# Kernel tuning notes

Hardware: AMD Instinct MI355X
Metric: run time of the kernel (lower is better)

## Reference

```python
import jax, jax.numpy as jnp
import numpy as np

EPS = 1e-12


def _sn(w, u):
    """One power-iteration step of spectral norm (eval mode: u not updated).
    w: [out, in] (1x1 conv weight viewed as matrix); u: [1, out].
    u/v are computed without gradient (torch no_grad), but sv = v W^T u^T
    carries gradient through w, matching the source.
    """
    v = u @ w  # [1, in]
    v = v / jnp.maximum(jnp.linalg.norm(v), EPS)
    v = jax.lax.stop_gradient(v)
    u2 = v @ w.T  # [1, out]
    u2 = u2 / jnp.maximum(jnp.linalg.norm(u2), EPS)
    u2 = jax.lax.stop_gradient(u2)
    sv = (v @ w.T @ u2.T)[0, 0]
    return w / sv


def _conv1x1(x, w):
    # x: [B,C,H,W], w: [O,C] -> [B,O,H,W]
    return jnp.einsum('oc,bchw->bohw', w, x)


def _maxpool2(x):
    B, C, H, W = x.shape
    return x.reshape(B, C, H // 2, 2, W // 2, 2).max(axis=(3, 5))


def setup_inputs() -> dict:
    key = jax.random.key(0)
    ks = jax.random.split(key, 10)
    B, C, H, W = 8, 512, 64, 64
    return {
        'x': jax.random.normal(ks[0], (B, C, H, W), jnp.float32),
        'w_theta': jax.random.normal(ks[1], (C // 8, C), jnp.float32) * 0.05,
        'w_phi': jax.random.normal(ks[2], (C // 8, C), jnp.float32) * 0.05,
        'w_g': jax.random.normal(ks[3], (C // 2, C), jnp.float32) * 0.05,
        'w_o': jax.random.normal(ks[4], (C, C // 2), jnp.float32) * 0.05,
        'u_theta': jax.random.normal(ks[5], (1, C // 8), jnp.float32),
        'u_phi': jax.random.normal(ks[6], (1, C // 8), jnp.float32),
        'u_g': jax.random.normal(ks[7], (1, C // 2), jnp.float32),
        'u_o': jax.random.normal(ks[8], (1, C), jnp.float32),
        'gamma': jax.random.normal(ks[9], (), jnp.float32),
    }


def reference(x, w_theta, w_phi, w_g, w_o, u_theta, u_phi, u_g, u_o, gamma):
    B, C, H, W = x.shape
    theta = _conv1x1(x, _sn(w_theta, u_theta))               # [B, C/8, H, W]
    phi = _maxpool2(_conv1x1(x, _sn(w_phi, u_phi)))          # [B, C/8, H/2, W/2]
    g = _maxpool2(_conv1x1(x, _sn(w_g, u_g)))                # [B, C/2, H/2, W/2]
    theta = theta.reshape(B, C // 8, H * W)
    phi = phi.reshape(B, C // 8, H * W // 4)
    g = g.reshape(B, C // 2, H * W // 4)
    # attention: [B, HW, HW/4]
    beta = jax.nn.softmax(jnp.einsum('bcn,bcm->bnm', theta, phi), axis=-1)
    o = jnp.einsum('bcm,bnm->bcn', g, beta).reshape(B, C // 2, H, W)
    o = _conv1x1(o, _sn(w_o, u_o))                           # [B, C, H, W]
    return gamma * o + x
```

## Files before the change

kernel.cpp:

```cpp
#include <hip/hip_runtime.h>
#include <math.h>

#define NB 8
#define NC 512
#define CK 64
#define CG 256
#define NPIX 4096
#define MPIX 1024

#define OFF_WT 0u
#define OFF_WP 32768u
#define OFF_WG 65536u
#define OFF_WO 196608u
#define OFF_TH 327680u
#define OFF_PH 2424832u
#define OFF_G  2949120u
#define OFF_OA 5046272u

__global__ __launch_bounds__(256) void sn_kernel(
    const float* __restrict__ w_theta, const float* __restrict__ w_phi,
    const float* __restrict__ w_g, const float* __restrict__ w_o,
    const float* __restrict__ u_theta, const float* __restrict__ u_phi,
    const float* __restrict__ u_g, const float* __restrict__ u_o,
    float* __restrict__ ws) {
  const int which = blockIdx.x;
  const float* w; const float* u; int outn, inn; float* dst;
  if (which == 0)      { w = w_theta; u = u_theta; outn = 64;  inn = 512; dst = ws + OFF_WT; }
  else if (which == 1) { w = w_phi;   u = u_phi;   outn = 64;  inn = 512; dst = ws + OFF_WP; }
  else if (which == 2) { w = w_g;     u = u_g;     outn = 256; inn = 512; dst = ws + OFF_WG; }
  else                 { w = w_o;     u = u_o;     outn = 512; inn = 256; dst = ws + OFF_WO; }
  __shared__ float us[512];
  __shared__ float vs[512];
  __shared__ float red[256];
  const int t = threadIdx.x;
  for (int i = t; i < outn; i += 256) us[i] = u[i];
  __syncthreads();
  float v0 = 0.f, v1 = 0.f;
  const int i0 = t, i1 = t + 256;
  for (int o = 0; o < outn; ++o) {
    const float* wr = w + (size_t)o * inn;
    const float uo = us[o];
    v0 += uo * wr[i0];
    if (i1 < inn) v1 += uo * wr[i1];
  }
  float ss = v0 * v0 + ((i1 < inn) ? v1 * v1 : 0.f);
  red[t] = ss;
  __syncthreads();
  for (int s2 = 128; s2 > 0; s2 >>= 1) { if (t < s2) red[t] += red[t + s2]; __syncthreads(); }
  const float vnorm = fmaxf(sqrtf(red[0]), 1e-12f);
  const float vinv = 1.f / vnorm;
  vs[i0] = v0 * vinv;
  if (i1 < inn) vs[i1] = v1 * vinv;
  __syncthreads();
  float ss2 = 0.f;
  for (int o = t; o < outn; o += 256) {
    const float* wr = w + (size_t)o * inn;
    float s = 0.f;
    for (int i = 0; i < inn; ++i) s += wr[i] * vs[i];
    ss2 += s * s;
  }
  red[t] = ss2;
  __syncthreads();
  for (int s2 = 128; s2 > 0; s2 >>= 1) { if (t < s2) red[t] += red[t + s2]; __syncthreads(); }
  const float sv = fmaxf(sqrtf(red[0]), 1e-12f);
  const float inv = 1.f / sv;
  const int total = outn * inn;
  for (int k = t; k < total; k += 256) dst[k] = w[k] * inv;
}

__global__ __launch_bounds__(256) void qkv_gemm(
    const float* __restrict__ x, const float* __restrict__ wcat,
    float* __restrict__ th_out, float* __restrict__ ph_out, float* __restrict__ g_out) {
  const int b = blockIdx.z;
  const int m0 = blockIdx.y * 128;
  const int n0 = blockIdx.x * 128;
  const int t = threadIdx.x;
  const int tx = t & 15, ty = t >> 4;
  __shared__ float As[16][128];
  __shared__ float Bs[16][128];
  float acc[8][8];
#pragma unroll
  for (int r = 0; r < 8; ++r)
#pragma unroll
    for (int j = 0; j < 8; ++j) acc[r][j] = 0.f;
  const float* xb = x + (size_t)b * NC * NPIX;
  const int am = t >> 1, ak = (t & 1) * 8;
  const int bk = t >> 4, bn = (t & 15) * 8;
  const float* aptr = wcat + (size_t)(m0 + am) * 512 + ak;
  const float* bptr = xb + (size_t)bk * NPIX + n0 + bn;
  float4 a0 = *(const float4*)(aptr);
  float4 a1 = *(const float4*)(aptr + 4);
  float4 b0 = *(const float4*)(bptr);
  float4 b1 = *(const float4*)(bptr + 4);
  for (int k0 = 0; k0 < 512; k0 += 16) {
    __syncthreads();
    As[ak + 0][am] = a0.x; As[ak + 1][am] = a0.y; As[ak + 2][am] = a0.z; As[ak + 3][am] = a0.w;
    As[ak + 4][am] = a1.x; As[ak + 5][am] = a1.y; As[ak + 6][am] = a1.z; As[ak + 7][am] = a1.w;
    *(float4*)&Bs[bk][bn] = b0;
    *(float4*)&Bs[bk][bn + 4] = b1;
    __syncthreads();
    if (k0 + 16 < 512) {
      a0 = *(const float4*)(aptr + k0 + 16);
      a1 = *(const float4*)(aptr + k0 + 20);
      b0 = *(const float4*)(bptr + (size_t)(k0 + 16) * NPIX);
      b1 = *(const float4*)(bptr + (size_t)(k0 + 16) * NPIX + 4);
    }
#pragma unroll
    for (int kk = 0; kk < 16; ++kk) {
      float4 av0 = *(float4*)&As[kk][ty * 4];
      float4 av1 = *(float4*)&As[kk][ty * 4 + 64];
      float4 bv0 = *(float4*)&Bs[kk][tx * 4];
      float4 bv1 = *(float4*)&Bs[kk][tx * 4 + 64];
      float a[8] = {av0.x, av0.y, av0.z, av0.w, av1.x, av1.y, av1.z, av1.w};
      float bb[8] = {bv0.x, bv0.y, bv0.z, bv0.w, bv1.x, bv1.y, bv1.z, bv1.w};
#pragma unroll
      for (int r = 0; r < 8; ++r)
#pragma unroll
        for (int j = 0; j < 8; ++j) acc[r][j] = fmaf(a[r], bb[j], acc[r][j]);
    }
  }
  const int hp = n0 >> 7;
#pragma unroll
  for (int r = 0; r < 8; ++r) {
    const int ch = m0 + ty * 4 + (r & 3) + ((r >= 4) ? 64 : 0);
    if (ch < 64) {
      float4 v0 = {acc[r][0], acc[r][1], acc[r][2], acc[r][3]};
      float4 v1 = {acc[r][4], acc[r][5], acc[r][6], acc[r][7]};
      float* dst = th_out + ((size_t)(b * CK + ch)) * NPIX + n0;
      *(float4*)(dst + tx * 4) = v0;
      *(float4*)(dst + 64 + tx * 4) = v1;
    } else {
      const float p0 = fmaxf(fmaxf(acc[r][0], acc[r][1]), fmaxf(acc[r][4], acc[r][5]));
      const float p1 = fmaxf(fmaxf(acc[r][2], acc[r][3]), fmaxf(acc[r][6], acc[r][7]));
      float* dst;
      if (ch < 128) dst = ph_out + ((size_t)(b * CK + (ch - 64))) * MPIX + hp * 32 + tx * 2;
      else          dst = g_out  + ((size_t)(b * CG + (ch - 128))) * MPIX + hp * 32 + tx * 2;
      float2 pv = {p0, p1};
      *(float2*)dst = pv;
    }
  }
}

__global__ __launch_bounds__(256) void attn_kernel(
    const float* __restrict__ th, const float* __restrict__ ph,
    const float* __restrict__ gg, float* __restrict__ oat) {
  const int b = blockIdx.x & 7;
  const int n0 = (blockIdx.x >> 3) * 64;
  const int t = threadIdx.x;
  const int tx = t & 15, tg = t >> 4;
  __shared__ float sth[64][64];
  __shared__ float buf[2][64][64];
  __shared__ float seb[64][64];
  __shared__ float sden[64];
  {
    const float* src = th + (size_t)b * CK * NPIX + n0;
    for (int idx = t; idx < 1024; idx += 256) {
      int c = idx >> 4, q = (idx & 15) << 2;
      *(float4*)&sth[c][q] = *(const float4*)(src + (size_t)c * NPIX + q);
    }
  }
  const float* phb = ph + (size_t)b * CK * MPIX;
  const float* ggb = gg + (size_t)b * CG * MPIX;
  const int c0 = t >> 4;
  const int q0 = (t & 15) << 2;
  float4 rg[4];

#define LDTILE(KK) do {                                                        \
    const int k_ = (KK);                                                       \
    const int m0_ = (k_ / 5) * 64;                                             \
    const int sub_ = k_ - (k_ / 5) * 5;                                        \
    const float* src_ = (sub_ == 0) ? (phb + m0_)                              \
                       : (ggb + (size_t)(sub_ - 1) * 64 * MPIX + m0_);         \
    _Pragma("unroll")                                                          \
    for (int i_ = 0; i_ < 4; ++i_)                                             \
      rg[i_] = *(const float4*)(src_ + (size_t)(c0 + 16 * i_) * MPIX + q0);    \
  } while (0)

#define WRTILE(CUR, SWZ) do {                                                  \
    _Pragma("unroll")                                                          \
    for (int i_ = 0; i_ < 4; ++i_) {                                           \
      const int c_ = c0 + 16 * i_;                                             \
      const int q_ = (SWZ) ? (q0 ^ (((c_ >> 2) & 7) << 2)) : q0;               \
      *(float4*)&buf[CUR][c_][q_] = rg[i_];                                    \
    }                                                                          \
  } while (0)

  float num[4][4][4];
#pragma unroll
  for (int a = 0; a < 4; ++a)
#pragma unroll
    for (int r = 0; r < 4; ++r)
#pragma unroll
      for (int j = 0; j < 4; ++j) num[a][r][j] = 0.f;
  float denp[4] = {0.f, 0.f, 0.f, 0.f};
  const int swe = (tg & 7) << 2;
  const int swr = (tx & 7) << 2;
  const int swg = (tg & 7) << 2;

  LDTILE(0);
  WRTILE(0, 0);
  LDTILE(1);
  __syncthreads();

  for (int m0i = 0; m0i < 16; ++m0i) {
    const int kq = m0i * 5;
    const int curq = kq & 1;
    {
      float s[4][4];
#pragma unroll
      for (int r = 0; r < 4; ++r)
#pragma unroll
        for (int j = 0; j < 4; ++j) s[r][j] = 0.f;
#pragma unroll 16
      for (int c = 0; c < 64; ++c) {
        float4 av = *(float4*)&sth[c][4 * tg];
        float4 bv = *(float4*)&buf[curq][c][4 * tx];
        float a[4] = {av.x, av.y, av.z, av.w};
        float bb[4] = {bv.x, bv.y, bv.z, bv.w};
#pragma unroll
        for (int r = 0; r < 4; ++r)
#pragma unroll
          for (int j = 0; j < 4; ++j) s[r][j] = fmaf(a[r], bb[j], s[r][j]);
      }
#pragma unroll
      for (int r = 0; r < 4; ++r) {
        float e0 = __expf(fminf(s[r][0], 80.f));
        float e1 = __expf(fminf(s[r][1], 80.f));
        float e2 = __expf(fminf(s[r][2], 80.f));
        float e3 = __expf(fminf(s[r][3], 80.f));
        denp[r] += (e0 + e1) + (e2 + e3);
        float4 ev = {e0, e1, e2, e3};
        *(float4*)&seb[4 * tg + r][(4 * tx) ^ swe] = ev;
      }
    }
    __syncthreads();
    WRTILE(curq ^ 1, 1);
    LDTILE(kq + 2);
    __syncthreads();
#pragma unroll
    for (int cc = 0; cc < 4; ++cc) {
      const int kk = kq + 1 + cc;
      const int curk = kk & 1;
#pragma unroll 4
      for (int m4 = 0; m4 < 64; m4 += 4) {
        float gvf[4][4], evf[4][4];
#pragma unroll
        for (int r = 0; r < 4; ++r) {
          float4 gv = *(float4*)&buf[curk][4 * tg + r][m4 ^ swg];
          gvf[r][0] = gv.x; gvf[r][1] = gv.y; gvf[r][2] = gv.z; gvf[r][3] = gv.w;
        }
#pragma unroll
        for (int j = 0; j < 4; ++j) {
          float4 evv = *(float4*)&seb[4 * tx + j][m4 ^ swr];
          evf[j][0] = evv.x; evf[j][1] = evv.y; evf[j][2] = evv.z; evf[j][3] = evv.w;
        }
#pragma unroll
        for (int r = 0; r < 4; ++r)
#pragma unroll
          for (int j = 0; j < 4; ++j)
#pragma unroll
            for (int i = 0; i < 4; ++i)
              num[cc][r][j] = fmaf(gvf[r][i], evf[j][i], num[cc][r][j]);
      }
      __syncthreads();
      if (kk < 79) {
        WRTILE(curk ^ 1, cc != 3);
        if (kk < 78) LDTILE(kk + 2);
        __syncthreads();
      }
    }
  }
#undef LDTILE
#undef WRTILE
#pragma unroll
  for (int r = 0; r < 4; ++r) {
    float v = denp[r];
    v += __shfl_xor(v, 1, 16);
    v += __shfl_xor(v, 2, 16);
    v += __shfl_xor(v, 4, 16);
    v += __shfl_xor(v, 8, 16);
    denp[r] = v;
  }
  if (tx == 0) {
    sden[4 * tg + 0] = denp[0];
    sden[4 * tg + 1] = denp[1];
    sden[4 * tg + 2] = denp[2];
    sden[4 * tg + 3] = denp[3];
  }
  __syncthreads();
  float4 dv = *(float4*)&sden[4 * tx];
  float4 inv = {1.f / dv.x, 1.f / dv.y, 1.f / dv.z, 1.f / dv.w};
#pragma unroll
  for (int cc = 0; cc < 4; ++cc)
#pragma unroll
    for (int r = 0; r < 4; ++r) {
      float4 v = {num[cc][r][0] * inv.x, num[cc][r][1] * inv.y,
                  num[cc][r][2] * inv.z, num[cc][r][3] * inv.w};
      *(float4*)(oat + (size_t)(b * CG + cc * 64 + 4 * tg + r) * NPIX + n0 + 4 * tx) = v;
    }
}

__global__ __launch_bounds__(256) void out_gemm(
    const float* __restrict__ oat, const float* __restrict__ wo,
    const float* __restrict__ x, const float* __restrict__ gamma,
    float* __restrict__ out) {
  const int b = blockIdx.z;
  const int m0 = blockIdx.y * 128;
  const int n0 = blockIdx.x * 128;
  const int t = threadIdx.x;
  const int tx = t & 15, ty = t >> 4;
  __shared__ float As[16][128];
  __shared__ float Bs[16][128];
  float acc[8][8];
#pragma unroll
  for (int r = 0; r < 8; ++r)
#pragma unroll
    for (int j = 0; j < 8; ++j) acc[r][j] = 0.f;
  const float* ob = oat + (size_t)b * CG * NPIX;
  const int am = t >> 1, ak = (t & 1) * 8;
  const int bk = t >> 4, bn = (t & 15) * 8;
  const float* aptr = wo + (size_t)(m0 + am) * 256 + ak;
  const float* bptr = ob + (size_t)bk * NPIX + n0 + bn;
  float4 a0 = *(const float4*)(aptr);
  float4 a1 = *(const float4*)(aptr + 4);
  float4 b0 = *(const float4*)(bptr);
  float4 b1 = *(const float4*)(bptr + 4);
  for (int k0 = 0; k0 < 256; k0 += 16) {
    __syncthreads();
    As[ak + 0][am] = a0.x; As[ak + 1][am] = a0.y; As[ak + 2][am] = a0.z; As[ak + 3][am] = a0.w;
    As[ak + 4][am] = a1.x; As[ak + 5][am] = a1.y; As[ak + 6][am] = a1.z; As[ak + 7][am] = a1.w;
    *(float4*)&Bs[bk][bn] = b0;
    *(float4*)&Bs[bk][bn + 4] = b1;
    __syncthreads();
    if (k0 + 16 < 256) {
      a0 = *(const float4*)(aptr + k0 + 16);
      a1 = *(const float4*)(aptr + k0 + 20);
      b0 = *(const float4*)(bptr + (size_t)(k0 + 16) * NPIX);
      b1 = *(const float4*)(bptr + (size_t)(k0 + 16) * NPIX + 4);
    }
#pragma unroll
    for (int kk = 0; kk < 16; ++kk) {
      float4 av0 = *(float4*)&As[kk][ty * 4];
      float4 av1 = *(float4*)&As[kk][ty * 4 + 64];
      float4 bv0 = *(float4*)&Bs[kk][tx * 4];
      float4 bv1 = *(float4*)&Bs[kk][tx * 4 + 64];
      float a[8] = {av0.x, av0.y, av0.z, av0.w, av1.x, av1.y, av1.z, av1.w};
      float bb[8] = {bv0.x, bv0.y, bv0.z, bv0.w, bv1.x, bv1.y, bv1.z, bv1.w};
#pragma unroll
      for (int r = 0; r < 8; ++r)
#pragma unroll
        for (int j = 0; j < 8; ++j) acc[r][j] = fmaf(a[r], bb[j], acc[r][j]);
    }
  }
  const float gm = gamma[0];
#pragma unroll
  for (int r = 0; r < 8; ++r) {
    const int ch = m0 + ty * 4 + (r & 3) + ((r >= 4) ? 64 : 0);
    const size_t off = ((size_t)(b * NC + ch)) * NPIX + n0;
    const float* xs = x + off;
    float* dst = out + off;
    float4 x0 = *(const float4*)(xs + tx * 4);
    float4 x1 = *(const float4*)(xs + 64 + tx * 4);
    float4 v0 = {fmaf(gm, acc[r][0], x0.x), fmaf(gm, acc[r][1], x0.y),
                 fmaf(gm, acc[r][2], x0.z), fmaf(gm, acc[r][3], x0.w)};
    float4 v1 = {fmaf(gm, acc[r][4], x1.x), fmaf(gm, acc[r][5], x1.y),
                 fmaf(gm, acc[r][6], x1.z), fmaf(gm, acc[r][7], x1.w)};
    *(float4*)(dst + tx * 4) = v0;
    *(float4*)(dst + 64 + tx * 4) = v1;
  }
}

extern "C" void kernel_launch(void* const* d_in, const int* in_sizes, int n_in,
                              void* d_out, int out_size, void* d_ws, size_t ws_size,
                              hipStream_t stream) {
  (void)in_sizes; (void)n_in; (void)out_size; (void)ws_size;
  const float* x       = (const float*)d_in[0];
  const float* w_theta = (const float*)d_in[1];
  const float* w_phi   = (const float*)d_in[2];
  const float* w_g     = (const float*)d_in[3];
  const float* w_o     = (const float*)d_in[4];
  const float* u_theta = (const float*)d_in[5];
  const float* u_phi   = (const float*)d_in[6];
  const float* u_g     = (const float*)d_in[7];
  const float* u_o     = (const float*)d_in[8];
  const float* gamma   = (const float*)d_in[9];
  float* out = (float*)d_out;
  float* ws  = (float*)d_ws;

  sn_kernel<<<4, 256, 0, stream>>>(w_theta, w_phi, w_g, w_o,
                                   u_theta, u_phi, u_g, u_o, ws);
  qkv_gemm<<<dim3(32, 3, NB), 256, 0, stream>>>(x, ws + OFF_WT,
                                                ws + OFF_TH, ws + OFF_PH, ws + OFF_G);
  attn_kernel<<<512, 256, 0, stream>>>(ws + OFF_TH, ws + OFF_PH,
                                       ws + OFF_G, ws + OFF_OA);
  out_gemm<<<dim3(32, 4, NB), 256, 0, stream>>>(ws + OFF_OA, ws + OFF_WO,
                                                x, gamma, out);
}
```

Before: 1.022 ms.

## Split attention kernel over g-channel halves and single-buffer tiles for occupancy

The attention kernel now splits the 256 g channels into two halves across twice as many blocks. Each block recomputes the QK scores and exponentials for its half. The shared buffer drops from double to single buffering and the accumulators halve, which lowers register and LDS use so three blocks can fit per CU. The cost is duplicated score and exp work plus an extra barrier per tile. The exp argument is also shifted by a constant to reduce overflow risk.

```diff
diff --git a/kernel.cpp b/kernel.cpp
--- a/kernel.cpp
+++ b/kernel.cpp
@@ -141,15 +141,18 @@
   }
 }
 
-__global__ __launch_bounds__(256) void attn_kernel(
+__global__ __launch_bounds__(256, 3) void attn_kernel(
     const float* __restrict__ th, const float* __restrict__ ph,
     const float* __restrict__ gg, float* __restrict__ oat) {
-  const int b = blockIdx.x & 7;
-  const int n0 = (blockIdx.x >> 3) * 64;
+  const int bid = blockIdx.x;
+  const int b = bid & 7;
+  const int rr = bid >> 3;
+  const int n0 = (rr & 63) * 64;
+  const int half = rr >> 6;
   const int t = threadIdx.x;
   const int tx = t & 15, tg = t >> 4;
   __shared__ float sth[64][64];
-  __shared__ float buf[2][64][64];
+  __shared__ float buf[64][64];
   __shared__ float seb[64][64];
   __shared__ float sden[64];
   {
@@ -160,15 +163,15 @@
     }
   }
   const float* phb = ph + (size_t)b * CK * MPIX;
-  const float* ggb = gg + (size_t)b * CG * MPIX;
+  const float* ggb = gg + (size_t)(b * CG + half * 128) * MPIX;
   const int c0 = t >> 4;
   const int q0 = (t & 15) << 2;
   float4 rg[4];
 
 #define LDTILE(KK) do {                                                        \
     const int k_ = (KK);                                                       \
-    const int m0_ = (k_ / 5) * 64;                                             \
-    const int sub_ = k_ - (k_ / 5) * 5;                                        \
+    const int m0_ = (k_ / 3) * 64;                                             \
+    const int sub_ = k_ - (k_ / 3) * 3;                                        \
     const float* src_ = (sub_ == 0) ? (phb + m0_)                              \
                        : (ggb + (size_t)(sub_ - 1) * 64 * MPIX + m0_);         \
     _Pragma("unroll")                                                          \
@@ -176,18 +179,18 @@
       rg[i_] = *(const float4*)(src_ + (size_t)(c0 + 16 * i_) * MPIX + q0);    \
   } while (0)
 
-#define WRTILE(CUR, SWZ) do {                                                  \
+#define WRTILE(SWZ) do {                                                       \
     _Pragma("unroll")                                                          \
     for (int i_ = 0; i_ < 4; ++i_) {                                           \
       const int c_ = c0 + 16 * i_;                                             \
       const int q_ = (SWZ) ? (q0 ^ (((c_ >> 2) & 7) << 2)) : q0;               \
-      *(float4*)&buf[CUR][c_][q_] = rg[i_];                                    \
+      *(float4*)&buf[c_][q_] = rg[i_];                                         \
     }                                                                          \
   } while (0)
 
-  float num[4][4][4];
-#pragma unroll
-  for (int a = 0; a < 4; ++a)
+  float num[2][4][4];
+#pragma unroll
+  for (int a = 0; a < 2; ++a)
 #pragma unroll
     for (int r = 0; r < 4; ++r)
 #pragma unroll
@@ -198,14 +201,14 @@
   const int swg = (tg & 7) << 2;
 
   LDTILE(0);
-  WRTILE(0, 0);
-  LDTILE(1);
-  __syncthreads();
-
-  for (int m0i = 0; m0i < 16; ++m0i) {
-    const int kq = m0i * 5;
-    const int curq = kq & 1;
-    {
+
+  for (int k = 0; k < 48; ++k) {
+    const int sub = k - (k / 3) * 3;
+    __syncthreads();
+    WRTILE(sub != 0);
+    if (k < 47) LDTILE(k + 1);
+    __syncthreads();
+    if (sub == 0) {
       float s[4][4];
 #pragma unroll
       for (int r = 0; r < 4; ++r)
@@ -214,7 +217,7 @@
 #pragma unroll 16
       for (int c = 0; c < 64; ++c) {
         float4 av = *(float4*)&sth[c][4 * tg];
-        float4 bv = *(float4*)&buf[curq][c][4 * tx];
+        float4 bv = *(float4*)&buf[c][4 * tx];
         float a[4] = {av.x, av.y, av.z, av.w};
         float bb[4] = {bv.x, bv.y, bv.z, bv.w};
 #pragma unroll
@@ -224,29 +227,22 @@
       }
 #pragma unroll
       for (int r = 0; r < 4; ++r) {
-        float e0 = __expf(fminf(s[r][0], 80.f));
-        float e1 = __expf(fminf(s[r][1], 80.f));
-        float e2 = __expf(fminf(s[r][2], 80.f));
-        float e3 = __expf(fminf(s[r][3], 80.f));
+        float e0 = __expf(fminf(s[r][0] - 40.f, 80.f));
+        float e1 = __expf(fminf(s[r][1] - 40.f, 80.f));
+        float e2 = __expf(fminf(s[r][2] - 40.f, 80.f));
+        float e3 = __expf(fminf(s[r][3] - 40.f, 80.f));
         denp[r] += (e0 + e1) + (e2 + e3);
         float4 ev = {e0, e1, e2, e3};
         *(float4*)&seb[4 * tg + r][(4 * tx) ^ swe] = ev;
       }
-    }
-    __syncthreads();
-    WRTILE(curq ^ 1, 1);
-    LDTILE(kq + 2);
-    __syncthreads();
-#pragma unroll
-    for (int cc = 0; cc < 4; ++cc) {
-      const int kk = kq + 1 + cc;
-      const int curk = kk & 1;
+    } else {
+      const int cc = sub - 1;
 #pragma unroll 4
       for (int m4 = 0; m4 < 64; m4 += 4) {
         float gvf[4][4], evf[4][4];
 #pragma unroll
         for (int r = 0; r < 4; ++r) {
-          float4 gv = *(float4*)&buf[curk][4 * tg + r][m4 ^ swg];
+          float4 gv = *(float4*)&buf[4 * tg + r][m4 ^ swg];
           gvf[r][0] = gv.x; gvf[r][1] = gv.y; gvf[r][2] = gv.z; gvf[r][3] = gv.w;
         }
 #pragma unroll
@@ -261,12 +257,6 @@
 #pragma unroll
             for (int i = 0; i < 4; ++i)
               num[cc][r][j] = fmaf(gvf[r][i], evf[j][i], num[cc][r][j]);
-      }
-      __syncthreads();
-      if (kk < 79) {
-        WRTILE(curk ^ 1, cc != 3);
-        if (kk < 78) LDTILE(kk + 2);
-        __syncthreads();
       }
     }
   }
@@ -281,6 +271,7 @@
     v += __shfl_xor(v, 8, 16);
     denp[r] = v;
   }
+  __syncthreads();
   if (tx == 0) {
     sden[4 * tg + 0] = denp[0];
     sden[4 * tg + 1] = denp[1];
@@ -291,12 +282,13 @@
   float4 dv = *(float4*)&sden[4 * tx];
   float4 inv = {1.f / dv.x, 1.f / dv.y, 1.f / dv.z, 1.f / dv.w};
 #pragma unroll
-  for (int cc = 0; cc < 4; ++cc)
+  for (int cc = 0; cc < 2; ++cc)
 #pragma unroll
     for (int r = 0; r < 4; ++r) {
       float4 v = {num[cc][r][0] * inv.x, num[cc][r][1] * inv.y,
                   num[cc][r][2] * inv.z, num[cc][r][3] * inv.w};
-      *(float4*)(oat + (size_t)(b * CG + cc * 64 + 4 * tg + r) * NPIX + n0 + 4 * tx) = v;
+      *(float4*)(oat + (size_t)(b * CG + half * 128 + cc * 64 + 4 * tg + r) * NPIX
+                 + n0 + 4 * tx) = v;
     }
 }
 
@@ -391,8 +383,8 @@
                                    u_theta, u_phi, u_g, u_o, ws);
   qkv_gemm<<<dim3(32, 3, NB), 256, 0, stream>>>(x, ws + OFF_WT,
                                                 ws + OFF_TH, ws + OFF_PH, ws + OFF_G);
-  attn_kernel<<<512, 256, 0, stream>>>(ws + OFF_TH, ws + OFF_PH,
-                                       ws + OFF_G, ws + OFF_OA);
+  attn_kernel<<<1024, 256, 0, stream>>>(ws + OFF_TH, ws + OFF_PH,
+                                        ws + OFF_G, ws + OFF_OA);
   out_gemm<<<dim3(32, 4, NB), 256, 0, stream>>>(ws + OFF_OA, ws + OFF_WO,
                                                 x, gamma, out);
 }
```

New measurement: 975.7 us. 1.05x faster.
